# Performance work log

Measured on AMD Instinct MI355X. Metric: run time of the kernel, lower is better.

## Reference

```python
import math
import jax, jax.numpy as jnp
import numpy as np
from jax import lax

CELL = 8
BINS = 9


def setup_inputs() -> dict:
    key = jax.random.key(0)
    x = jax.random.uniform(key, (64, 3, 224, 224), dtype=jnp.float32)
    return {"x": x}


def reference(x):
    N, C, H, W = x.shape
    # Fixed Sobel buffers: one output channel summing over all input channels.
    sob = jnp.array([[-1.0, 0.0, 1.0], [-2.0, 0.0, 2.0], [-1.0, 0.0, 1.0]], dtype=x.dtype)
    kx = jnp.broadcast_to(sob, (1, C, 3, 3))          # SobelX weight [O=1, I=C, 3, 3]
    ky = jnp.broadcast_to(sob.T, (1, C, 3, 3))        # SobelY weight
    dn = ('NCHW', 'OIHW', 'NCHW')
    gx = lax.conv_general_dilated(x, kx, (1, 1), 'SAME', dimension_numbers=dn)  # [N,1,H,W]
    gy = lax.conv_general_dilated(x, ky, (1, 1), 'SAME', dimension_numbers=dn)
    mag = jnp.sqrt(gx * gx + gy * gy)                 # [N,1,H,W]
    ang = jnp.abs(jnp.arctan2(gx, gy))                # unsigned gradients -> [0, pi]
    bin_idx = jnp.floor(ang / math.pi * (BINS - 1)).astype(jnp.int32)  # [N,1,H,W], values in [0, BINS-1]
    # scatter_(1, bin_idx, mag) == one-hot along bin axis times magnitude
    onehot = (bin_idx == jnp.arange(BINS, dtype=jnp.int32)[None, :, None, None]).astype(x.dtype)  # [N,BINS,H,W]
    vol = onehot * mag                                # broadcast over bin axis
    # AvgPool2d(cell) * cell^2 == per-cell sum
    hog = vol.reshape(N, BINS, H // CELL, CELL, W // CELL, CELL).sum(axis=(3, 5))  # [N,BINS,H/8,W/8]
    return hog.reshape(N, -1)
```

## Files before the change

### kernel.cpp

```cpp
#include <hip/hip_runtime.h>
#include <math.h>


namespace {
constexpr int Himg = 224;
constexpr int Wimg = 224;
constexpr int NCELL = 28;
constexpr int BINS  = 9;
constexpr int ROWS  = 10;
constexpr int LDSW  = 232;

__global__ __launch_bounds__(256) void hog_kernel(const float* __restrict__ x,
                                                  float* __restrict__ out) {
    const int n  = blockIdx.y;
    const int cr = blockIdx.x;
    const int t  = threadIdx.x;

    __shared__ float s[ROWS][LDSW];
    __shared__ float h2[Wimg * BINS];

    if (t < ROWS * 8) {
        int r = t >> 3;
        int c = t & 7;
        int col = (c < 4) ? c : (224 + c);
        s[r][col] = 0.0f;
    }

    const int h0 = cr * 8 - 1;
    const float* xb = x + (size_t)n * 3 * Himg * Wimg;

    for (int idx = t; idx < ROWS * 56; idx += 256) {
        int r = idx / 56;
        int q = idx - r * 56;
        int w = q * 4;
        int h = h0 + r;
        float4 v = make_float4(0.f, 0.f, 0.f, 0.f);
        if (h >= 0 && h < Himg) {
            const float* r0 = xb + (size_t)h * Wimg;
            const float* r1 = r0 + Himg * Wimg;
            const float* r2 = r1 + Himg * Wimg;
            float4 a = *(const float4*)(r0 + w);
            float4 b = *(const float4*)(r1 + w);
            float4 c4 = *(const float4*)(r2 + w);
            v.x = a.x + b.x + c4.x;
            v.y = a.y + b.y + c4.y;
            v.z = a.z + b.z + c4.z;
            v.w = a.w + b.w + c4.w;
        }
        *(float4*)&s[r][4 + w] = v;
    }
    __syncthreads();

    const float PI_F = 3.14159265358979323846f;
    const float CK[8] = {0.92387953f, 0.70710678f, 0.38268343f, 0.0f,
                         -0.38268343f, -0.70710678f, -0.92387953f, -1.0f};

    if (t < Wimg) {
        const int w = t;
        float ml = s[0][3 + w], mc = s[0][4 + w], mr = s[0][5 + w];
        float zl = s[1][3 + w], zc = s[1][4 + w], zr = s[1][5 + w];
        float acc[BINS];
#pragma unroll
        for (int j = 0; j < BINS; ++j) acc[j] = 0.0f;

#pragma unroll
        for (int i = 0; i < 8; ++i) {
            float pl = s[i + 2][3 + w];
            float pc = s[i + 2][4 + w];
            float pr = s[i + 2][5 + w];

            float gx = (mr - ml) + 2.0f * (zr - zl) + (pr - pl);
            float gy = (pl + 2.0f * pc + pr) - (ml + 2.0f * mc + mr);
            float mag = sqrtf(gx * gx + gy * gy);

            float negy = -gy;
            int bin = 0;
            float guard = 1e30f;
#pragma unroll
            for (int j = 0; j < 8; ++j) {
                float sj = fmaf(mag, CK[j], negy);
                bin += (sj >= 0.0f) ? 1 : 0;
                guard = fminf(guard, fabsf(sj));
            }
            if (guard < mag * 1e-4f) {
                float ang = fabsf(atan2f(gx, gy));
                bin = (int)(ang / PI_F * 8.0f);
                bin = bin > 8 ? 8 : bin;
            }
#pragma unroll
            for (int j = 0; j < BINS; ++j) acc[j] += (bin == j) ? mag : 0.0f;

            ml = zl; mc = zc; mr = zr;
            zl = pl; zc = pc; zr = pr;
        }
#pragma unroll
        for (int j = 0; j < BINS; ++j) h2[w * BINS + j] = acc[j];
    }
    __syncthreads();

    if (t < NCELL * BINS) {
        int bin = t / NCELL;
        int cw  = t - bin * NCELL;
        float v = 0.0f;
#pragma unroll
        for (int c = 0; c < 8; ++c) v += h2[(cw * 8 + c) * BINS + bin];
        out[((size_t)n * BINS + bin) * (NCELL * NCELL) + (size_t)cr * NCELL + cw] = v;
    }
}
}

extern "C" void kernel_launch(void* const* d_in, const int* in_sizes, int n_in,
                              void* d_out, int out_size, void* d_ws, size_t ws_size,
                              hipStream_t stream) {
    const float* x = (const float*)d_in[0];
    float* out = (float*)d_out;
    const int N = in_sizes[0] / (3 * Himg * Wimg);
    dim3 grid(NCELL, N);
    hog_kernel<<<grid, 256, 0, stream>>>(x, out);
}
```

Measured before the change: 83.83 us.

## Process two cell rows per block with 512 threads and batched loads

Each block now covers 16 image rows (two cell rows) using 512 threads, loading 18 halo rows instead of 10 twice. This cuts the redundant halo reads from 25% to about 12.5% and halves the number of blocks. Global loads are issued together into registers before the LDS stores, which gives more memory-level parallelism. The cost is a larger LDS footprint per block and fewer blocks in total (896), which may lower occupancy or load balance.

```diff
diff --git a/kernel.cpp b/kernel.cpp
--- a/kernel.cpp
+++ b/kernel.cpp
@@ -7,17 +7,18 @@
 constexpr int Wimg = 224;
 constexpr int NCELL = 28;
 constexpr int BINS  = 9;
-constexpr int ROWS  = 10;
+constexpr int ROWS  = 18;
 constexpr int LDSW  = 232;
+constexpr int NCHUNK = ROWS * 56;
 
-__global__ __launch_bounds__(256) void hog_kernel(const float* __restrict__ x,
+__global__ __launch_bounds__(512) void hog_kernel(const float* __restrict__ x,
                                                   float* __restrict__ out) {
     const int n  = blockIdx.y;
-    const int cr = blockIdx.x;
+    const int pr = blockIdx.x;
     const int t  = threadIdx.x;
 
     __shared__ float s[ROWS][LDSW];
-    __shared__ float h2[Wimg * BINS];
+    __shared__ float h2[448 * BINS];
 
     if (t < ROWS * 8) {
         int r = t >> 3;
@@ -26,51 +27,64 @@
         s[r][col] = 0.0f;
     }
 
-    const int h0 = cr * 8 - 1;
+    const int h0 = pr * 16 - 1;
     const float* xb = x + (size_t)n * 3 * Himg * Wimg;
 
-    for (int idx = t; idx < ROWS * 56; idx += 256) {
-        int r = idx / 56;
+    float4 va[2];
+    int    lofs[2];
+    bool   act[2];
+#pragma unroll
+    for (int k = 0; k < 2; ++k) {
+        int idx = t + 512 * k;
+        bool pred = idx < NCHUNK;
+        int r = pred ? (idx / 56) : 0;
         int q = idx - r * 56;
         int w = q * 4;
         int h = h0 + r;
+        act[k]  = pred;
+        lofs[k] = r * LDSW + 4 + w;
         float4 v = make_float4(0.f, 0.f, 0.f, 0.f);
-        if (h >= 0 && h < Himg) {
-            const float* r0 = xb + (size_t)h * Wimg;
-            const float* r1 = r0 + Himg * Wimg;
-            const float* r2 = r1 + Himg * Wimg;
-            float4 a = *(const float4*)(r0 + w);
-            float4 b = *(const float4*)(r1 + w);
-            float4 c4 = *(const float4*)(r2 + w);
+        if (pred && h >= 0 && h < Himg) {
+            const float* r0 = xb + (size_t)h * Wimg + w;
+            float4 a = *(const float4*)(r0);
+            float4 b = *(const float4*)(r0 + Himg * Wimg);
+            float4 c4 = *(const float4*)(r0 + 2 * Himg * Wimg);
             v.x = a.x + b.x + c4.x;
             v.y = a.y + b.y + c4.y;
             v.z = a.z + b.z + c4.z;
             v.w = a.w + b.w + c4.w;
         }
-        *(float4*)&s[r][4 + w] = v;
+        va[k] = v;
     }
+#pragma unroll
+    for (int k = 0; k < 2; ++k)
+        if (act[k]) *(float4*)&((float*)s)[lofs[k]] = va[k];
     __syncthreads();
 
     const float PI_F = 3.14159265358979323846f;
     const float CK[8] = {0.92387953f, 0.70710678f, 0.38268343f, 0.0f,
                          -0.38268343f, -0.70710678f, -0.92387953f, -1.0f};
 
-    if (t < Wimg) {
-        const int w = t;
-        float ml = s[0][3 + w], mc = s[0][4 + w], mr = s[0][5 + w];
-        float zl = s[1][3 + w], zc = s[1][4 + w], zr = s[1][5 + w];
+    if (t < 448) {
+        const int g = t >> 5 >= 7 ? 1 : 0;
+        const int gg = t / 224;
+        const int w  = t - gg * 224;
+        (void)g;
+        const int rb = gg * 8;
+        float ml = s[rb][3 + w], mc = s[rb][4 + w], mr = s[rb][5 + w];
+        float zl = s[rb + 1][3 + w], zc = s[rb + 1][4 + w], zr = s[rb + 1][5 + w];
         float acc[BINS];
 #pragma unroll
         for (int j = 0; j < BINS; ++j) acc[j] = 0.0f;
 
 #pragma unroll
         for (int i = 0; i < 8; ++i) {
-            float pl = s[i + 2][3 + w];
-            float pc = s[i + 2][4 + w];
-            float pr = s[i + 2][5 + w];
+            float pl = s[rb + i + 2][3 + w];
+            float pc = s[rb + i + 2][4 + w];
+            float pr2 = s[rb + i + 2][5 + w];
 
-            float gx = (mr - ml) + 2.0f * (zr - zl) + (pr - pl);
-            float gy = (pl + 2.0f * pc + pr) - (ml + 2.0f * mc + mr);
+            float gx = (mr - ml) + 2.0f * (zr - zl) + (pr2 - pl);
+            float gy = (pl + 2.0f * pc + pr2) - (ml + 2.0f * mc + mr);
             float mag = sqrtf(gx * gx + gy * gy);
 
             float negy = -gy;
@@ -91,19 +105,23 @@
             for (int j = 0; j < BINS; ++j) acc[j] += (bin == j) ? mag : 0.0f;
 
             ml = zl; mc = zc; mr = zr;
-            zl = pl; zc = pc; zr = pr;
+            zl = pl; zc = pc; zr = pr2;
         }
 #pragma unroll
-        for (int j = 0; j < BINS; ++j) h2[w * BINS + j] = acc[j];
+        for (int j = 0; j < BINS; ++j) h2[t * BINS + j] = acc[j];
     }
     __syncthreads();
 
-    if (t < NCELL * BINS) {
-        int bin = t / NCELL;
-        int cw  = t - bin * NCELL;
+    if (t < 2 * NCELL * BINS) {
+        int grp = t / (NCELL * BINS);
+        int rem = t - grp * (NCELL * BINS);
+        int bin = rem / NCELL;
+        int cw  = rem - bin * NCELL;
+        int cr  = pr * 2 + grp;
         float v = 0.0f;
 #pragma unroll
-        for (int c = 0; c < 8; ++c) v += h2[(cw * 8 + c) * BINS + bin];
+        for (int c = 0; c < 8; ++c)
+            v += h2[(grp * 224 + cw * 8 + c) * BINS + bin];
         out[((size_t)n * BINS + bin) * (NCELL * NCELL) + (size_t)cr * NCELL + cw] = v;
     }
 }
@@ -115,6 +133,6 @@
     const float* x = (const float*)d_in[0];
     float* out = (float*)d_out;
     const int N = in_sizes[0] / (3 * Himg * Wimg);
-    dim3 grid(NCELL, N);
-    hog_kernel<<<grid, 256, 0, stream>>>(x, out);
+    dim3 grid(NCELL / 2, N);
+    hog_kernel<<<grid, 512, 0, stream>>>(x, out);
 }
```

New measurement: 83.49 us. About the same (-0.4%).
